# Kernel optimization log

Hardware: AMD Instinct MI355X
Metric: run time of the kernel (lower is better)

Reference implementation:

```python
import jax, jax.numpy as jnp
import numpy as np

B, MSG, H, D, N = 64, 64, 512, 512, 2048


def setup_inputs() -> dict:
    key = jax.random.key(0)
    ks = jax.random.split(key, 20)
    s = 0.02
    return {
        "message": jax.random.normal(ks[0], (B, MSG), jnp.float32),
        "state": jax.random.normal(ks[1], (B, H), jnp.float32),
        "image": jax.random.normal(ks[2], (B, H), jnp.float32),
        "class_descriptors": jax.random.normal(ks[3], (N, D), jnp.float32),
        # GRUCell params (torch layout: gates ordered r, z, n)
        "w_ih": jax.random.normal(ks[4], (3 * H, MSG), jnp.float32) * s,
        "w_hh": jax.random.normal(ks[5], (3 * H, H), jnp.float32) * s,
        "b_ih": jax.random.normal(ks[6], (3 * H,), jnp.float32) * s,
        "b_hh": jax.random.normal(ks[7], (3 * H,), jnp.float32) * s,
        "w_stop": jax.random.normal(ks[8], (1, H), jnp.float32) * s,
        "b_stop": jax.random.normal(ks[9], (1,), jnp.float32) * s,
        "w_y1": jax.random.normal(ks[10], (H, H + D), jnp.float32) * s,
        "b_y1": jax.random.normal(ks[11], (H,), jnp.float32) * s,
        "w_y2": jax.random.normal(ks[12], (1, H), jnp.float32) * s,
        "b_y2": jax.random.normal(ks[13], (1,), jnp.float32) * s,
        "w_state": jax.random.normal(ks[14], (H, H), jnp.float32) * s,
        "b_state": jax.random.normal(ks[15], (H,), jnp.float32) * s,
        "w_desc": jax.random.normal(ks[16], (H, D), jnp.float32) * s,  # no bias
        "w_msg": jax.random.normal(ks[17], (MSG, H), jnp.float32) * s,
        "b_msg": jax.random.normal(ks[18], (MSG,), jnp.float32) * s,
    }


def _gru_cell(x, h, w_ih, w_hh, b_ih, b_hh):
    gi = x @ w_ih.T + b_ih  # [B, 3H]
    gh = h @ w_hh.T + b_hh
    i_r, i_z, i_n = jnp.split(gi, 3, axis=1)
    h_r, h_z, h_n = jnp.split(gh, 3, axis=1)
    r = jax.nn.sigmoid(i_r + h_r)
    z = jax.nn.sigmoid(i_z + h_z)
    n = jnp.tanh(i_n + r * h_n)
    return (1.0 - z) * n + z * h


def reference(message, state, image, class_descriptors,
              w_ih, w_hh, b_ih, b_hh, w_stop, b_stop,
              w_y1, b_y1, w_y2, b_y2, w_state, b_state,
              w_desc, w_msg, b_msg):
    b, h = state.shape
    n, d = class_descriptors.shape

    new_state = _gru_cell(message, state, w_ih, w_hh, b_ih, b_hh)  # [B, H]
    stop_dist = jax.nn.sigmoid(new_state @ w_stop.T + b_stop)  # [B, 1]
    stop_bit = jax.lax.stop_gradient(jnp.round(stop_dist))  # eval-mode path

    # build_state_descriptor_pairs (faithful to torch view semantics,
    # including the (B, H, N) -> (B*N, H) interleaved reshape of pair_left)
    pair_left = jnp.broadcast_to(new_state[:, :, None], (b, h, n)).reshape(b * n, h)
    pair_right = jnp.broadcast_to(class_descriptors[None], (b, n, d)).reshape(b * n, d)
    pairs = jnp.concatenate([pair_left, pair_right], axis=1)  # [B*N, H+D]

    y = jnp.clip(pairs @ w_y1.T + b_y1, 0.0, None)  # relu, [B*N, H]
    y = (y @ w_y2.T + b_y2).reshape(b, -1)  # [B, N]
    y_scores = jax.lax.stop_gradient(jax.nn.softmax(y, axis=1))

    # reweight_descriptors: softmax-weighted sum over descriptors
    descriptor_influence = jnp.einsum('bn,nd->bd', y_scores, class_descriptors)

    message_state = jnp.tanh(new_state @ w_state.T + b_state
                             + descriptor_influence @ w_desc.T)
    message_dist = jax.nn.sigmoid(message_state @ w_msg.T + b_msg)  # [B, MSG]
    outp_msg = jax.lax.stop_gradient(jnp.round(message_dist))

    return stop_bit, stop_dist, outp_msg, message_dist, y
```

## Files before the change

kernel.cpp:

```cpp
#include <hip/hip_runtime.h>
#include <hip/hip_bf16.h>


__device__ __forceinline__ float sigm(float x) { return 1.0f / (1.0f + expf(-x)); }

__device__ __forceinline__ void stage_pad68(float* dst, const float* src, int c) {
  *(float4*)&dst[(c >> 4) * 68 + (c & 15) * 4] = *(const float4*)&src[c * 4];
}

__global__ __launch_bounds__(512) void gru_kernel(
    const float* __restrict__ msg, const float* __restrict__ st,
    const float* __restrict__ w_ih, const float* __restrict__ w_hh,
    const float* __restrict__ b_ih, const float* __restrict__ b_hh,
    float* __restrict__ ns, float* __restrict__ nsT) {
  const int h = blockIdx.x;
  const int t = threadIdx.x;
  __shared__ __align__(16) float sHr[544], sHz[544], sHn[544];
  __shared__ __align__(16) float sIr[64], sIz[64], sIn[64];
  if (t < 128)      stage_pad68(sHr, w_hh + h * 512, t);
  else if (t < 256) stage_pad68(sHz, w_hh + (h + 512) * 512, t - 128);
  else if (t < 384) stage_pad68(sHn, w_hh + (h + 1024) * 512, t - 256);
  else if (t < 400) ((float4*)sIr)[t - 384] = ((const float4*)(w_ih + h * 64))[t - 384];
  else if (t < 416) ((float4*)sIz)[t - 400] = ((const float4*)(w_ih + (h + 512) * 64))[t - 400];
  else if (t < 432) ((float4*)sIn)[t - 416] = ((const float4*)(w_ih + (h + 1024) * 64))[t - 416];
  __syncthreads();
  const int bi = t >> 3, kg = t & 7;
  float pr = 0.f, pz = 0.f, pin = 0.f, phn = 0.f;
  {
    const float* mrow = msg + bi * 64 + kg * 8;
    const float* ir = &sIr[kg * 8];
    const float* iz = &sIz[kg * 8];
    const float* in_ = &sIn[kg * 8];
    #pragma unroll
    for (int i = 0; i < 2; ++i) {
      float4 x = *(const float4*)&mrow[i * 4];
      float4 wr = *(const float4*)&ir[i * 4];
      float4 wz = *(const float4*)&iz[i * 4];
      float4 wn = *(const float4*)&in_[i * 4];
      pr = fmaf(x.x, wr.x, pr); pr = fmaf(x.y, wr.y, pr); pr = fmaf(x.z, wr.z, pr); pr = fmaf(x.w, wr.w, pr);
      pz = fmaf(x.x, wz.x, pz); pz = fmaf(x.y, wz.y, pz); pz = fmaf(x.z, wz.z, pz); pz = fmaf(x.w, wz.w, pz);
      pin = fmaf(x.x, wn.x, pin); pin = fmaf(x.y, wn.y, pin); pin = fmaf(x.z, wn.z, pin); pin = fmaf(x.w, wn.w, pin);
    }
  }
  {
    const float* srow = st + bi * 512 + kg * 64;
    const float* hr = &sHr[kg * 68];
    const float* hz = &sHz[kg * 68];
    const float* hn = &sHn[kg * 68];
    #pragma unroll
    for (int i = 0; i < 16; ++i) {
      float4 x = *(const float4*)&srow[i * 4];
      float4 wr = *(const float4*)&hr[i * 4];
      float4 wz = *(const float4*)&hz[i * 4];
      float4 wn = *(const float4*)&hn[i * 4];
      pr = fmaf(x.x, wr.x, pr); pr = fmaf(x.y, wr.y, pr); pr = fmaf(x.z, wr.z, pr); pr = fmaf(x.w, wr.w, pr);
      pz = fmaf(x.x, wz.x, pz); pz = fmaf(x.y, wz.y, pz); pz = fmaf(x.z, wz.z, pz); pz = fmaf(x.w, wz.w, pz);
      phn = fmaf(x.x, wn.x, phn); phn = fmaf(x.y, wn.y, phn); phn = fmaf(x.z, wn.z, phn); phn = fmaf(x.w, wn.w, phn);
    }
  }
  pr += __shfl_xor(pr, 1, 8); pr += __shfl_xor(pr, 2, 8); pr += __shfl_xor(pr, 4, 8);
  pz += __shfl_xor(pz, 1, 8); pz += __shfl_xor(pz, 2, 8); pz += __shfl_xor(pz, 4, 8);
  pin += __shfl_xor(pin, 1, 8); pin += __shfl_xor(pin, 2, 8); pin += __shfl_xor(pin, 4, 8);
  phn += __shfl_xor(phn, 1, 8); phn += __shfl_xor(phn, 2, 8); phn += __shfl_xor(phn, 4, 8);
  if ((t & 7) == 0) {
    float r = sigm(pr + b_ih[h] + b_hh[h]);
    float z = sigm(pz + b_ih[h + 512] + b_hh[h + 512]);
    float n = tanhf(pin + b_ih[h + 1024] + r * (phn + b_hh[h + 1024]));
    float hp = st[bi * 512 + h];
    float v = (1.0f - z) * n + z * hp;
    ns[bi * 512 + h] = v;
    nsT[h * 64 + bi] = v;
  }
}

__global__ __launch_bounds__(512) void stopws1_kernel(
    const float* __restrict__ w_y1, float* __restrict__ ws1,
    const float* __restrict__ ns, const float* __restrict__ w_stop,
    const float* __restrict__ b_stop, float* __restrict__ out_bit,
    float* __restrict__ out_dist) {
  const int t = threadIdx.x;
  if (blockIdx.x < 64) {
    const int j = blockIdx.x * 8 + (t >> 6);
    const int lane = t & 63;
    const float* row = w_y1 + j * 1024 + lane * 8;
    float4 a = *(const float4*)&row[0];
    float4 b = *(const float4*)&row[4];
    float acc = a.x + a.y + a.z + a.w + b.x + b.y + b.z + b.w;
    #pragma unroll
    for (int m = 1; m < 64; m <<= 1) acc += __shfl_xor(acc, m, 64);
    if (lane == 0) ws1[j] = acc;
  } else {
    const int bi = t >> 3, kg = t & 7;
    const float* row = ns + bi * 512 + kg * 64;
    const float* wrow = w_stop + kg * 64;
    float acc = 0.f;
    #pragma unroll
    for (int i = 0; i < 16; ++i) {
      float4 r = *(const float4*)&row[i * 4];
      float4 w = *(const float4*)&wrow[i * 4];
      acc = fmaf(r.x, w.x, acc); acc = fmaf(r.y, w.y, acc);
      acc = fmaf(r.z, w.z, acc); acc = fmaf(r.w, w.w, acc);
    }
    acc += __shfl_xor(acc, 1, 8); acc += __shfl_xor(acc, 2, 8); acc += __shfl_xor(acc, 4, 8);
    if ((t & 7) == 0) {
      float sd = sigm(acc + b_stop[0]);
      out_dist[bi] = sd;
      out_bit[bi] = rintf(sd);
    }
  }
}

#define GBK 16
__global__ __launch_bounds__(256) void g_kernel(
    const float* __restrict__ desc, const float* __restrict__ w_y1,
    const float* __restrict__ b_y1, const float* __restrict__ nsT,
    const float* __restrict__ ws1, const float* __restrict__ w_y2,
    float* __restrict__ yp) {
  __shared__ __align__(16) float As[GBK][64];
  __shared__ __align__(16) float Bs[GBK][64];
  __shared__ __align__(16) float sV[16][66];
  __shared__ __align__(16) float sW1[64], sW2[64];
  const int rr0 = blockIdx.x * 64;
  const int j0 = blockIdx.y * 64;
  const int tid = threadIdx.x;
  const int tm = (tid >> 4) * 4;
  const int tn = (tid & 15) * 4;
  const int lm = tid >> 2;
  const int lkq = (tid & 3) * 4;
  {
    const int q = tid >> 4, pos = (tid & 15) * 4;
    *(float4*)&sV[q][pos] = *(const float4*)&nsT[((rr0 >> 2) + q) * 64 + pos];
  }
  if (tid < 64) { sW1[tid] = ws1[j0 + tid]; sW2[tid] = w_y2[j0 + tid]; }
  float acc[4][4] = {};
  const float* aptr = desc + (rr0 + lm) * 512 + lkq;
  const float* bptr = w_y1 + (j0 + lm) * 1024 + 512 + lkq;
  float4 av = *(const float4*)aptr;
  float4 bv = *(const float4*)bptr;
  for (int k0 = 0; k0 < 512; k0 += GBK) {
    __syncthreads();
    As[lkq + 0][lm] = av.x; As[lkq + 1][lm] = av.y;
    As[lkq + 2][lm] = av.z; As[lkq + 3][lm] = av.w;
    Bs[lkq + 0][lm] = bv.x; Bs[lkq + 1][lm] = bv.y;
    Bs[lkq + 2][lm] = bv.z; Bs[lkq + 3][lm] = bv.w;
    __syncthreads();
    if (k0 + GBK < 512) {
      av = *(const float4*)(aptr + k0 + GBK);
      bv = *(const float4*)(bptr + k0 + GBK);
    }
    #pragma unroll
    for (int k = 0; k < GBK; ++k) {
      float4 a = *(const float4*)&As[k][tm];
      float4 b = *(const float4*)&Bs[k][tn];
      acc[0][0] = fmaf(a.x, b.x, acc[0][0]); acc[0][1] = fmaf(a.x, b.y, acc[0][1]);
      acc[0][2] = fmaf(a.x, b.z, acc[0][2]); acc[0][3] = fmaf(a.x, b.w, acc[0][3]);
      acc[1][0] = fmaf(a.y, b.x, acc[1][0]); acc[1][1] = fmaf(a.y, b.y, acc[1][1]);
      acc[1][2] = fmaf(a.y, b.z, acc[1][2]); acc[1][3] = fmaf(a.y, b.w, acc[1][3]);
      acc[2][0] = fmaf(a.z, b.x, acc[2][0]); acc[2][1] = fmaf(a.z, b.y, acc[2][1]);
      acc[2][2] = fmaf(a.z, b.z, acc[2][2]); acc[2][3] = fmaf(a.z, b.w, acc[2][3]);
      acc[3][0] = fmaf(a.w, b.x, acc[3][0]); acc[3][1] = fmaf(a.w, b.y, acc[3][1]);
      acc[3][2] = fmaf(a.w, b.z, acc[3][2]); acc[3][3] = fmaf(a.w, b.w, acc[3][3]);
    }
  }
  {
    float4 by = *(const float4*)&b_y1[j0 + tn];
    #pragma unroll
    for (int i = 0; i < 4; ++i) {
      acc[i][0] += by.x; acc[i][1] += by.y; acc[i][2] += by.z; acc[i][3] += by.w;
    }
  }
  const float4 w1 = *(const float4*)&sW1[tn];
  const float4 w2 = *(const float4*)&sW2[tn];
  const int vrow = tid >> 4;
  float* ypb = yp + blockIdx.y * 131072 + rr0 + tm;
  for (int bi = 0; bi < 64; ++bi) {
    const float v = sV[vrow][bi];
    float p0 = fmaf(w2.x, fmaxf(fmaf(v, w1.x, acc[0][0]), 0.f),
               fmaf(w2.y, fmaxf(fmaf(v, w1.y, acc[0][1]), 0.f),
               fmaf(w2.z, fmaxf(fmaf(v, w1.z, acc[0][2]), 0.f),
                    w2.w * fmaxf(fmaf(v, w1.w, acc[0][3]), 0.f))));
    float p1 = fmaf(w2.x, fmaxf(fmaf(v, w1.x, acc[1][0]), 0.f),
               fmaf(w2.y, fmaxf(fmaf(v, w1.y, acc[1][1]), 0.f),
               fmaf(w2.z, fmaxf(fmaf(v, w1.z, acc[1][2]), 0.f),
                    w2.w * fmaxf(fmaf(v, w1.w, acc[1][3]), 0.f))));
    float p2 = fmaf(w2.x, fmaxf(fmaf(v, w1.x, acc[2][0]), 0.f),
               fmaf(w2.y, fmaxf(fmaf(v, w1.y, acc[2][1]), 0.f),
               fmaf(w2.z, fmaxf(fmaf(v, w1.z, acc[2][2]), 0.f),
                    w2.w * fmaxf(fmaf(v, w1.w, acc[2][3]), 0.f))));
    float p3 = fmaf(w2.x, fmaxf(fmaf(v, w1.x, acc[3][0]), 0.f),
               fmaf(w2.y, fmaxf(fmaf(v, w1.y, acc[3][1]), 0.f),
               fmaf(w2.z, fmaxf(fmaf(v, w1.z, acc[3][2]), 0.f),
                    w2.w * fmaxf(fmaf(v, w1.w, acc[3][3]), 0.f))));
    p0 += __shfl_xor(p0, 1, 16); p0 += __shfl_xor(p0, 2, 16); p0 += __shfl_xor(p0, 4, 16); p0 += __shfl_xor(p0, 8, 16);
    p1 += __shfl_xor(p1, 1, 16); p1 += __shfl_xor(p1, 2, 16); p1 += __shfl_xor(p1, 4, 16); p1 += __shfl_xor(p1, 8, 16);
    p2 += __shfl_xor(p2, 1, 16); p2 += __shfl_xor(p2, 2, 16); p2 += __shfl_xor(p2, 4, 16); p2 += __shfl_xor(p2, 8, 16);
    p3 += __shfl_xor(p3, 1, 16); p3 += __shfl_xor(p3, 2, 16); p3 += __shfl_xor(p3, 4, 16); p3 += __shfl_xor(p3, 8, 16);
    if ((tid & 15) == 0) *(float4*)&ypb[bi * 2048] = make_float4(p0, p1, p2, p3);
  }
}

__global__ __launch_bounds__(256) void softmax_kernel(
    const float* __restrict__ yp, const float* __restrict__ b_y2,
    float* __restrict__ scores, float* __restrict__ out_y) {
  const int bi = blockIdx.x;
  const int t = threadIdx.x;
  __shared__ float sy[2048];
  __shared__ float red[256];
  const float b = b_y2[0];
  float lmax = -3.0e38f;
  for (int i = t; i < 2048; i += 256) {
    const float* p = yp + bi * 2048 + i;
    float v = b + p[0] + p[131072] + p[262144] + p[393216]
                + p[524288] + p[655360] + p[786432] + p[917504];
    sy[i] = v;
    out_y[bi * 2048 + i] = v;
    lmax = fmaxf(lmax, v);
  }
  red[t] = lmax;
  __syncthreads();
  for (int s = 128; s > 0; s >>= 1) {
    if (t < s) red[t] = fmaxf(red[t], red[t + s]);
    __syncthreads();
  }
  const float mx = red[0];
  __syncthreads();
  float lsum = 0.0f;
  for (int i = t; i < 2048; i += 256) {
    float e = expf(sy[i] - mx);
    sy[i] = e;
    lsum += e;
  }
  red[t] = lsum;
  __syncthreads();
  for (int s = 128; s > 0; s >>= 1) {
    if (t < s) red[t] += red[t + s];
    __syncthreads();
  }
  const float inv = 1.0f / red[0];
  for (int i = t; i < 2048; i += 256) scores[bi * 2048 + i] = sy[i] * inv;
}

__global__ __launch_bounds__(256) void di_part_kernel(
    const float* __restrict__ scores, const float* __restrict__ desc,
    float* __restrict__ dp) {
  __shared__ __align__(16) float sS[64][64];
  __shared__ __align__(16) float sD[64][64];
  const int d0 = blockIdx.x * 64;
  const int n0 = blockIdx.y * 64;
  const int tid = threadIdx.x;
  {
    const int bi = tid >> 2;
    #pragma unroll
    for (int i = 0; i < 4; ++i) {
      const int kq = (tid & 3) * 4 + i * 16;
      float4 av = *(const float4*)&scores[bi * 2048 + n0 + kq];
      sS[kq + 0][bi] = av.x; sS[kq + 1][bi] = av.y;
      sS[kq + 2][bi] = av.z; sS[kq + 3][bi] = av.w;
    }
  }
  {
    #pragma unroll
    for (int i = 0; i < 4; ++i) {
      const int nn = (tid >> 4) + i * 16;
      const int dq = (tid & 15) * 4;
      *(float4*)&sD[nn][dq] = *(const float4*)&desc[(n0 + nn) * 512 + d0 + dq];
    }
  }
  __syncthreads();
  const int bi0 = (tid >> 4) * 4;
  const int dd0 = (tid & 15) * 4;
  float acc[4][4] = {};
  #pragma unroll 8
  for (int nn = 0; nn < 64; ++nn) {
    float4 a = *(const float4*)&sS[nn][bi0];
    float4 b = *(const float4*)&sD[nn][dd0];
    acc[0][0] = fmaf(a.x, b.x, acc[0][0]); acc[0][1] = fmaf(a.x, b.y, acc[0][1]);
    acc[0][2] = fmaf(a.x, b.z, acc[0][2]); acc[0][3] = fmaf(a.x, b.w, acc[0][3]);
    acc[1][0] = fmaf(a.y, b.x, acc[1][0]); acc[1][1] = fmaf(a.y, b.y, acc[1][1]);
    acc[1][2] = fmaf(a.y, b.z, acc[1][2]); acc[1][3] = fmaf(a.y, b.w, acc[1][3]);
    acc[2][0] = fmaf(a.z, b.x, acc[2][0]); acc[2][1] = fmaf(a.z, b.y, acc[2][1]);
    acc[2][2] = fmaf(a.z, b.z, acc[2][2]); acc[2][3] = fmaf(a.z, b.w, acc[2][3]);
    acc[3][0] = fmaf(a.w, b.x, acc[3][0]); acc[3][1] = fmaf(a.w, b.y, acc[3][1]);
    acc[3][2] = fmaf(a.w, b.z, acc[3][2]); acc[3][3] = fmaf(a.w, b.w, acc[3][3]);
  }
  float* base = dp + blockIdx.y * 32768;
  #pragma unroll
  for (int i = 0; i < 4; ++i)
    #pragma unroll
    for (int j = 0; j < 4; ++j)
      base[(bi0 + i) * 512 + d0 + dd0 + j] = acc[i][j];
}

__global__ __launch_bounds__(512) void di_reduce_kernel(
    const float* __restrict__ dp, float* __restrict__ di) {
  const int idx = blockIdx.x * 512 + threadIdx.x;
  float acc = 0.0f;
  #pragma unroll 8
  for (int c = 0; c < 32; ++c) acc += dp[c * 32768 + idx];
  di[idx] = acc;
}

__global__ __launch_bounds__(512) void ms_kernel(
    const float* __restrict__ ns, const float* __restrict__ di,
    const float* __restrict__ w_state, const float* __restrict__ b_state,
    const float* __restrict__ w_desc, float* __restrict__ ms) {
  const int hj = blockIdx.x;
  const int t = threadIdx.x;
  __shared__ __align__(16) float sWs[544], sWd[544];
  if (t < 128)      stage_pad68(sWs, w_state + hj * 512, t);
  else if (t < 256) stage_pad68(sWd, w_desc + hj * 512, t - 128);
  __syncthreads();
  const int bi = t >> 3, kg = t & 7;
  const float* nr = ns + bi * 512 + kg * 64;
  const float* dr = di + bi * 512 + kg * 64;
  const float* wsp = &sWs[kg * 68];
  const float* wdp = &sWd[kg * 68];
  float acc = 0.f;
  #pragma unroll
  for (int i = 0; i < 16; ++i) {
    float4 a = *(const float4*)&nr[i * 4];
    float4 w = *(const float4*)&wsp[i * 4];
    float4 b = *(const float4*)&dr[i * 4];
    float4 u = *(const float4*)&wdp[i * 4];
    acc = fmaf(a.x, w.x, acc); acc = fmaf(a.y, w.y, acc);
    acc = fmaf(a.z, w.z, acc); acc = fmaf(a.w, w.w, acc);
    acc = fmaf(b.x, u.x, acc); acc = fmaf(b.y, u.y, acc);
    acc = fmaf(b.z, u.z, acc); acc = fmaf(b.w, u.w, acc);
  }
  acc += __shfl_xor(acc, 1, 8); acc += __shfl_xor(acc, 2, 8); acc += __shfl_xor(acc, 4, 8);
  if ((t & 7) == 0) ms[bi * 512 + hj] = tanhf(acc + b_state[hj]);
}

__global__ __launch_bounds__(512) void msg_kernel(
    const float* __restrict__ ms, const float* __restrict__ w_msg,
    const float* __restrict__ b_msg, float* __restrict__ out_msg,
    float* __restrict__ out_msgdist) {
  const int m = blockIdx.x;
  const int t = threadIdx.x;
  __shared__ __align__(16) float sW[544];
  if (t < 128) stage_pad68(sW, w_msg + m * 512, t);
  __syncthreads();
  const int bi = t >> 3, kg = t & 7;
  const float* row = ms + bi * 512 + kg * 64;
  const float* wp = &sW[kg * 68];
  float acc = 0.f;
  #pragma unroll
  for (int i = 0; i < 16; ++i) {
    float4 a = *(const float4*)&row[i * 4];
    float4 w = *(const float4*)&wp[i * 4];
    acc = fmaf(a.x, w.x, acc); acc = fmaf(a.y, w.y, acc);
    acc = fmaf(a.z, w.z, acc); acc = fmaf(a.w, w.w, acc);
  }
  acc += __shfl_xor(acc, 1, 8); acc += __shfl_xor(acc, 2, 8); acc += __shfl_xor(acc, 4, 8);
  if ((t & 7) == 0) {
    float md = sigm(acc + b_msg[m]);
    out_msgdist[bi * 64 + m] = md;
    out_msg[bi * 64 + m] = rintf(md);
  }
}

extern "C" void kernel_launch(void* const* d_in, const int* in_sizes, int n_in,
                              void* d_out, int out_size, void* d_ws, size_t ws_size,
                              hipStream_t stream) {
  (void)in_sizes; (void)n_in; (void)out_size; (void)ws_size;
  const float* message = (const float*)d_in[0];
  const float* state   = (const float*)d_in[1];
  const float* desc    = (const float*)d_in[3];
  const float* w_ih    = (const float*)d_in[4];
  const float* w_hh    = (const float*)d_in[5];
  const float* b_ih    = (const float*)d_in[6];
  const float* b_hh    = (const float*)d_in[7];
  const float* w_stop  = (const float*)d_in[8];
  const float* b_stop  = (const float*)d_in[9];
  const float* w_y1    = (const float*)d_in[10];
  const float* b_y1    = (const float*)d_in[11];
  const float* w_y2    = (const float*)d_in[12];
  const float* b_y2    = (const float*)d_in[13];
  const float* w_state = (const float*)d_in[14];
  const float* b_state = (const float*)d_in[15];
  const float* w_desc  = (const float*)d_in[16];
  const float* w_msg   = (const float*)d_in[17];
  const float* b_msg   = (const float*)d_in[18];

  float* out = (float*)d_out;
  float* out_stopbit  = out;
  float* out_stopdist = out + 64;
  float* out_msg      = out + 128;
  float* out_msgdist  = out + 4224;
  float* out_y        = out + 8320;

  char* ws = (char*)d_ws;
  float* ns     = (float*)(ws);
  float* nsT    = (float*)(ws + 131072);
  float* ws1    = (float*)(ws + 262144);
  float* yp     = (float*)(ws + 270336);
  float* scores = (float*)(ws + 4988928);
  float* di     = (float*)(ws + 5513216);
  float* ms     = (float*)(ws + 5644288);

  gru_kernel<<<512, 512, 0, stream>>>(message, state, w_ih, w_hh, b_ih, b_hh, ns, nsT);
  stopws1_kernel<<<65, 512, 0, stream>>>(w_y1, ws1, ns, w_stop, b_stop, out_stopbit, out_stopdist);
  g_kernel<<<dim3(32, 8), 256, 0, stream>>>(desc, w_y1, b_y1, nsT, ws1, w_y2, yp);
  softmax_kernel<<<64, 256, 0, stream>>>(yp, b_y2, scores, out_y);
  di_part_kernel<<<dim3(8, 32), 256, 0, stream>>>(scores, desc, yp);
  di_reduce_kernel<<<64, 512, 0, stream>>>(yp, di);
  ms_kernel<<<512, 512, 0, stream>>>(ns, di, w_state, b_state, w_desc, ms);
  msg_kernel<<<64, 512, 0, stream>>>(ms, w_msg, b_msg, out_msg, out_msgdist);
}
```

Measured before the change: 213.8 us.

## Fuse all stages into one persistent kernel with software grid barriers

Replaces the eight separate kernel launches with a single persistent 256-block kernel. The stages are separated by an atomic-counter grid barrier, and the barrier counter is reset each call with a memset. The goal is to remove launch gaps and per-kernel ramp-up. In exchange, phases that used 512 blocks now loop twice per block, the GEMM phase is retiled with 512 threads and its epilogue restructured, and correctness depends on all 256 blocks being co-resident.

```diff
diff --git a/kernel.cpp b/kernel.cpp
--- a/kernel.cpp
+++ b/kernel.cpp
@@ -1,6 +1,19 @@
 #include <hip/hip_runtime.h>
-#include <hip/hip_bf16.h>
-
+
+
+#define NBLK 256
+#define SMEM_FLOATS 9696
+
+struct Params {
+  const float *message, *state, *desc;
+  const float *w_ih, *w_hh, *b_ih, *b_hh;
+  const float *w_stop, *b_stop;
+  const float *w_y1, *b_y1, *w_y2, *b_y2;
+  const float *w_state, *b_state, *w_desc, *w_msg, *b_msg;
+  float *out_stopbit, *out_stopdist, *out_msg, *out_msgdist, *out_y;
+  float *ns, *nsT, *ws1, *yp, *scores, *di, *ms;
+  int *bar;
+};
 
 __device__ __forceinline__ float sigm(float x) { return 1.0f / (1.0f + expf(-x)); }
 
@@ -8,91 +21,108 @@
   *(float4*)&dst[(c >> 4) * 68 + (c & 15) * 4] = *(const float4*)&src[c * 4];
 }
 
-__global__ __launch_bounds__(512) void gru_kernel(
-    const float* __restrict__ msg, const float* __restrict__ st,
-    const float* __restrict__ w_ih, const float* __restrict__ w_hh,
-    const float* __restrict__ b_ih, const float* __restrict__ b_hh,
-    float* __restrict__ ns, float* __restrict__ nsT) {
-  const int h = blockIdx.x;
-  const int t = threadIdx.x;
-  __shared__ __align__(16) float sHr[544], sHz[544], sHn[544];
-  __shared__ __align__(16) float sIr[64], sIz[64], sIn[64];
-  if (t < 128)      stage_pad68(sHr, w_hh + h * 512, t);
-  else if (t < 256) stage_pad68(sHz, w_hh + (h + 512) * 512, t - 128);
-  else if (t < 384) stage_pad68(sHn, w_hh + (h + 1024) * 512, t - 256);
-  else if (t < 400) ((float4*)sIr)[t - 384] = ((const float4*)(w_ih + h * 64))[t - 384];
-  else if (t < 416) ((float4*)sIz)[t - 400] = ((const float4*)(w_ih + (h + 512) * 64))[t - 400];
-  else if (t < 432) ((float4*)sIn)[t - 416] = ((const float4*)(w_ih + (h + 1024) * 64))[t - 416];
-  __syncthreads();
-  const int bi = t >> 3, kg = t & 7;
-  float pr = 0.f, pz = 0.f, pin = 0.f, phn = 0.f;
-  {
-    const float* mrow = msg + bi * 64 + kg * 8;
-    const float* ir = &sIr[kg * 8];
-    const float* iz = &sIz[kg * 8];
-    const float* in_ = &sIn[kg * 8];
-    #pragma unroll
-    for (int i = 0; i < 2; ++i) {
-      float4 x = *(const float4*)&mrow[i * 4];
-      float4 wr = *(const float4*)&ir[i * 4];
-      float4 wz = *(const float4*)&iz[i * 4];
-      float4 wn = *(const float4*)&in_[i * 4];
-      pr = fmaf(x.x, wr.x, pr); pr = fmaf(x.y, wr.y, pr); pr = fmaf(x.z, wr.z, pr); pr = fmaf(x.w, wr.w, pr);
-      pz = fmaf(x.x, wz.x, pz); pz = fmaf(x.y, wz.y, pz); pz = fmaf(x.z, wz.z, pz); pz = fmaf(x.w, wz.w, pz);
-      pin = fmaf(x.x, wn.x, pin); pin = fmaf(x.y, wn.y, pin); pin = fmaf(x.z, wn.z, pin); pin = fmaf(x.w, wn.w, pin);
-    }
-  }
-  {
-    const float* srow = st + bi * 512 + kg * 64;
-    const float* hr = &sHr[kg * 68];
-    const float* hz = &sHz[kg * 68];
-    const float* hn = &sHn[kg * 68];
-    #pragma unroll
-    for (int i = 0; i < 16; ++i) {
-      float4 x = *(const float4*)&srow[i * 4];
-      float4 wr = *(const float4*)&hr[i * 4];
-      float4 wz = *(const float4*)&hz[i * 4];
-      float4 wn = *(const float4*)&hn[i * 4];
-      pr = fmaf(x.x, wr.x, pr); pr = fmaf(x.y, wr.y, pr); pr = fmaf(x.z, wr.z, pr); pr = fmaf(x.w, wr.w, pr);
-      pz = fmaf(x.x, wz.x, pz); pz = fmaf(x.y, wz.y, pz); pz = fmaf(x.z, wz.z, pz); pz = fmaf(x.w, wz.w, pz);
-      phn = fmaf(x.x, wn.x, phn); phn = fmaf(x.y, wn.y, phn); phn = fmaf(x.z, wn.z, phn); phn = fmaf(x.w, wn.w, phn);
-    }
-  }
-  pr += __shfl_xor(pr, 1, 8); pr += __shfl_xor(pr, 2, 8); pr += __shfl_xor(pr, 4, 8);
-  pz += __shfl_xor(pz, 1, 8); pz += __shfl_xor(pz, 2, 8); pz += __shfl_xor(pz, 4, 8);
-  pin += __shfl_xor(pin, 1, 8); pin += __shfl_xor(pin, 2, 8); pin += __shfl_xor(pin, 4, 8);
-  phn += __shfl_xor(phn, 1, 8); phn += __shfl_xor(phn, 2, 8); phn += __shfl_xor(phn, 4, 8);
-  if ((t & 7) == 0) {
-    float r = sigm(pr + b_ih[h] + b_hh[h]);
-    float z = sigm(pz + b_ih[h + 512] + b_hh[h + 512]);
-    float n = tanhf(pin + b_ih[h + 1024] + r * (phn + b_hh[h + 1024]));
-    float hp = st[bi * 512 + h];
-    float v = (1.0f - z) * n + z * hp;
-    ns[bi * 512 + h] = v;
-    nsT[h * 64 + bi] = v;
-  }
-}
-
-__global__ __launch_bounds__(512) void stopws1_kernel(
-    const float* __restrict__ w_y1, float* __restrict__ ws1,
-    const float* __restrict__ ns, const float* __restrict__ w_stop,
-    const float* __restrict__ b_stop, float* __restrict__ out_bit,
-    float* __restrict__ out_dist) {
-  const int t = threadIdx.x;
-  if (blockIdx.x < 64) {
-    const int j = blockIdx.x * 8 + (t >> 6);
+__device__ __forceinline__ void grid_barrier(int* bar) {
+  __syncthreads();
+  __threadfence();
+  if (threadIdx.x == 0) {
+    int* cnt = bar;
+    int* gen = bar + 1;
+    int g = __hip_atomic_load(gen, __ATOMIC_ACQUIRE, __HIP_MEMORY_SCOPE_AGENT);
+    int a = __hip_atomic_fetch_add(cnt, 1, __ATOMIC_ACQ_REL, __HIP_MEMORY_SCOPE_AGENT);
+    if (a == NBLK - 1) {
+      __hip_atomic_store(cnt, 0, __ATOMIC_RELAXED, __HIP_MEMORY_SCOPE_AGENT);
+      __hip_atomic_store(gen, g + 1, __ATOMIC_RELEASE, __HIP_MEMORY_SCOPE_AGENT);
+    } else {
+      while (__hip_atomic_load(gen, __ATOMIC_ACQUIRE, __HIP_MEMORY_SCOPE_AGENT) == g) {
+        __builtin_amdgcn_s_sleep(2);
+      }
+    }
+  }
+  __syncthreads();
+}
+
+__device__ void phase_gru(const Params& P, float* sm, int blk, int t) {
+  float* sHr = sm;
+  float* sHz = sm + 544;
+  float* sHn = sm + 1088;
+  float* sIr = sm + 1632;
+  float* sIz = sm + 1696;
+  float* sIn = sm + 1760;
+  for (int pass = 0; pass < 2; ++pass) {
+    const int h = blk + pass * 256;
+    __syncthreads();
+    if (t < 128)      stage_pad68(sHr, P.w_hh + h * 512, t);
+    else if (t < 256) stage_pad68(sHz, P.w_hh + (h + 512) * 512, t - 128);
+    else if (t < 384) stage_pad68(sHn, P.w_hh + (h + 1024) * 512, t - 256);
+    else if (t < 400) ((float4*)sIr)[t - 384] = ((const float4*)(P.w_ih + h * 64))[t - 384];
+    else if (t < 416) ((float4*)sIz)[t - 400] = ((const float4*)(P.w_ih + (h + 512) * 64))[t - 400];
+    else if (t < 432) ((float4*)sIn)[t - 416] = ((const float4*)(P.w_ih + (h + 1024) * 64))[t - 416];
+    __syncthreads();
+    const int bi = t >> 3, kg = t & 7;
+    float pr = 0.f, pz = 0.f, pin = 0.f, phn = 0.f;
+    {
+      const float* mrow = P.message + bi * 64 + kg * 8;
+      const float* ir = &sIr[kg * 8];
+      const float* iz = &sIz[kg * 8];
+      const float* in_ = &sIn[kg * 8];
+      #pragma unroll
+      for (int i = 0; i < 2; ++i) {
+        float4 x = *(const float4*)&mrow[i * 4];
+        float4 wr = *(const float4*)&ir[i * 4];
+        float4 wz = *(const float4*)&iz[i * 4];
+        float4 wn = *(const float4*)&in_[i * 4];
+        pr = fmaf(x.x, wr.x, pr); pr = fmaf(x.y, wr.y, pr); pr = fmaf(x.z, wr.z, pr); pr = fmaf(x.w, wr.w, pr);
+        pz = fmaf(x.x, wz.x, pz); pz = fmaf(x.y, wz.y, pz); pz = fmaf(x.z, wz.z, pz); pz = fmaf(x.w, wz.w, pz);
+        pin = fmaf(x.x, wn.x, pin); pin = fmaf(x.y, wn.y, pin); pin = fmaf(x.z, wn.z, pin); pin = fmaf(x.w, wn.w, pin);
+      }
+    }
+    {
+      const float* srow = P.state + bi * 512 + kg * 64;
+      const float* hr = &sHr[kg * 68];
+      const float* hz = &sHz[kg * 68];
+      const float* hn = &sHn[kg * 68];
+      #pragma unroll
+      for (int i = 0; i < 16; ++i) {
+        float4 x = *(const float4*)&srow[i * 4];
+        float4 wr = *(const float4*)&hr[i * 4];
+        float4 wz = *(const float4*)&hz[i * 4];
+        float4 wn = *(const float4*)&hn[i * 4];
+        pr = fmaf(x.x, wr.x, pr); pr = fmaf(x.y, wr.y, pr); pr = fmaf(x.z, wr.z, pr); pr = fmaf(x.w, wr.w, pr);
+        pz = fmaf(x.x, wz.x, pz); pz = fmaf(x.y, wz.y, pz); pz = fmaf(x.z, wz.z, pz); pz = fmaf(x.w, wz.w, pz);
+        phn = fmaf(x.x, wn.x, phn); phn = fmaf(x.y, wn.y, phn); phn = fmaf(x.z, wn.z, phn); phn = fmaf(x.w, wn.w, phn);
+      }
+    }
+    pr += __shfl_xor(pr, 1, 8); pr += __shfl_xor(pr, 2, 8); pr += __shfl_xor(pr, 4, 8);
+    pz += __shfl_xor(pz, 1, 8); pz += __shfl_xor(pz, 2, 8); pz += __shfl_xor(pz, 4, 8);
+    pin += __shfl_xor(pin, 1, 8); pin += __shfl_xor(pin, 2, 8); pin += __shfl_xor(pin, 4, 8);
+    phn += __shfl_xor(phn, 1, 8); phn += __shfl_xor(phn, 2, 8); phn += __shfl_xor(phn, 4, 8);
+    if ((t & 7) == 0) {
+      float r = sigm(pr + P.b_ih[h] + P.b_hh[h]);
+      float z = sigm(pz + P.b_ih[h + 512] + P.b_hh[h + 512]);
+      float n = tanhf(pin + P.b_ih[h + 1024] + r * (phn + P.b_hh[h + 1024]));
+      float hp = P.state[bi * 512 + h];
+      float v = (1.0f - z) * n + z * hp;
+      P.ns[bi * 512 + h] = v;
+      P.nsT[h * 64 + bi] = v;
+    }
+  }
+}
+
+__device__ void phase_stopws1(const Params& P, int blk, int t) {
+  if (blk < 64) {
+    const int j = blk * 8 + (t >> 6);
     const int lane = t & 63;
-    const float* row = w_y1 + j * 1024 + lane * 8;
+    const float* row = P.w_y1 + j * 1024 + lane * 8;
     float4 a = *(const float4*)&row[0];
     float4 b = *(const float4*)&row[4];
     float acc = a.x + a.y + a.z + a.w + b.x + b.y + b.z + b.w;
     #pragma unroll
     for (int m = 1; m < 64; m <<= 1) acc += __shfl_xor(acc, m, 64);
-    if (lane == 0) ws1[j] = acc;
-  } else {
+    if (lane == 0) P.ws1[j] = acc;
+  } else if (blk == 64) {
     const int bi = t >> 3, kg = t & 7;
-    const float* row = ns + bi * 512 + kg * 64;
-    const float* wrow = w_stop + kg * 64;
+    const float* row = P.ns + bi * 512 + kg * 64;
+    const float* wrow = P.w_stop + kg * 64;
     float acc = 0.f;
     #pragma unroll
     for (int i = 0; i < 16; ++i) {
@@ -103,245 +133,203 @@
     }
     acc += __shfl_xor(acc, 1, 8); acc += __shfl_xor(acc, 2, 8); acc += __shfl_xor(acc, 4, 8);
     if ((t & 7) == 0) {
-      float sd = sigm(acc + b_stop[0]);
-      out_dist[bi] = sd;
-      out_bit[bi] = rintf(sd);
-    }
-  }
-}
-
-#define GBK 16
-__global__ __launch_bounds__(256) void g_kernel(
-    const float* __restrict__ desc, const float* __restrict__ w_y1,
-    const float* __restrict__ b_y1, const float* __restrict__ nsT,
-    const float* __restrict__ ws1, const float* __restrict__ w_y2,
-    float* __restrict__ yp) {
-  __shared__ __align__(16) float As[GBK][64];
-  __shared__ __align__(16) float Bs[GBK][64];
-  __shared__ __align__(16) float sV[16][66];
-  __shared__ __align__(16) float sW1[64], sW2[64];
-  const int rr0 = blockIdx.x * 64;
-  const int j0 = blockIdx.y * 64;
-  const int tid = threadIdx.x;
-  const int tm = (tid >> 4) * 4;
-  const int tn = (tid & 15) * 4;
-  const int lm = tid >> 2;
-  const int lkq = (tid & 3) * 4;
-  {
-    const int q = tid >> 4, pos = (tid & 15) * 4;
-    *(float4*)&sV[q][pos] = *(const float4*)&nsT[((rr0 >> 2) + q) * 64 + pos];
-  }
-  if (tid < 64) { sW1[tid] = ws1[j0 + tid]; sW2[tid] = w_y2[j0 + tid]; }
-  float acc[4][4] = {};
-  const float* aptr = desc + (rr0 + lm) * 512 + lkq;
-  const float* bptr = w_y1 + (j0 + lm) * 1024 + 512 + lkq;
+      float sd = sigm(acc + P.b_stop[0]);
+      P.out_stopdist[bi] = sd;
+      P.out_stopbit[bi] = rintf(sd);
+    }
+  }
+}
+
+__device__ void phase_g(const Params& P, float* sm, int blk, int t) {
+  float* As  = sm;
+  float* Bs  = sm + 2176;
+  float* Gt  = sm + 4352;
+  float* sV  = sm + 8512;
+  float* sW1 = sm + 9568;
+  float* sW2 = sm + 9632;
+  const int rr0 = (blk >> 3) * 64;
+  const int j0  = (blk & 7) * 64;
+  if (t < 256) {
+    const int q = t >> 4, pos = (t & 15) * 4;
+    *(float4*)&sV[q * 66 + pos] = *(const float4*)&P.nsT[((rr0 >> 2) + q) * 64 + pos];
+  }
+  if (t < 64) { sW1[t] = P.ws1[j0 + t]; sW2[t] = P.w_y2[j0 + t]; }
+  const int lm = t >> 3, lk4 = (t & 7) * 4;
+  const int tm2 = (t >> 4) * 2;
+  const int tn4 = (t & 15) * 4;
+  const float* aptr = P.desc + (rr0 + lm) * 512 + lk4;
+  const float* bptr = P.w_y1 + (j0 + lm) * 1024 + 512 + lk4;
   float4 av = *(const float4*)aptr;
   float4 bv = *(const float4*)bptr;
-  for (int k0 = 0; k0 < 512; k0 += GBK) {
-    __syncthreads();
-    As[lkq + 0][lm] = av.x; As[lkq + 1][lm] = av.y;
-    As[lkq + 2][lm] = av.z; As[lkq + 3][lm] = av.w;
-    Bs[lkq + 0][lm] = bv.x; Bs[lkq + 1][lm] = bv.y;
-    Bs[lkq + 2][lm] = bv.z; Bs[lkq + 3][lm] = bv.w;
-    __syncthreads();
-    if (k0 + GBK < 512) {
-      av = *(const float4*)(aptr + k0 + GBK);
-      bv = *(const float4*)(bptr + k0 + GBK);
+  float acc[2][4] = {};
+  for (int k0 = 0; k0 < 512; k0 += 32) {
+    __syncthreads();
+    As[(lk4 + 0) * 68 + lm] = av.x; As[(lk4 + 1) * 68 + lm] = av.y;
+    As[(lk4 + 2) * 68 + lm] = av.z; As[(lk4 + 3) * 68 + lm] = av.w;
+    Bs[(lk4 + 0) * 68 + lm] = bv.x; Bs[(lk4 + 1) * 68 + lm] = bv.y;
+    Bs[(lk4 + 2) * 68 + lm] = bv.z; Bs[(lk4 + 3) * 68 + lm] = bv.w;
+    __syncthreads();
+    if (k0 + 32 < 512) {
+      av = *(const float4*)(aptr + k0 + 32);
+      bv = *(const float4*)(bptr + k0 + 32);
     }
     #pragma unroll
-    for (int k = 0; k < GBK; ++k) {
-      float4 a = *(const float4*)&As[k][tm];
-      float4 b = *(const float4*)&Bs[k][tn];
+    for (int k = 0; k < 32; ++k) {
+      float2 a = *(const float2*)&As[k * 68 + tm2];
+      float4 b = *(const float4*)&Bs[k * 68 + tn4];
       acc[0][0] = fmaf(a.x, b.x, acc[0][0]); acc[0][1] = fmaf(a.x, b.y, acc[0][1]);
       acc[0][2] = fmaf(a.x, b.z, acc[0][2]); acc[0][3] = fmaf(a.x, b.w, acc[0][3]);
       acc[1][0] = fmaf(a.y, b.x, acc[1][0]); acc[1][1] = fmaf(a.y, b.y, acc[1][1]);
       acc[1][2] = fmaf(a.y, b.z, acc[1][2]); acc[1][3] = fmaf(a.y, b.w, acc[1][3]);
-      acc[2][0] = fmaf(a.z, b.x, acc[2][0]); acc[2][1] = fmaf(a.z, b.y, acc[2][1]);
-      acc[2][2] = fmaf(a.z, b.z, acc[2][2]); acc[2][3] = fmaf(a.z, b.w, acc[2][3]);
-      acc[3][0] = fmaf(a.w, b.x, acc[3][0]); acc[3][1] = fmaf(a.w, b.y, acc[3][1]);
-      acc[3][2] = fmaf(a.w, b.z, acc[3][2]); acc[3][3] = fmaf(a.w, b.w, acc[3][3]);
     }
   }
   {
-    float4 by = *(const float4*)&b_y1[j0 + tn];
+    float4 by = *(const float4*)&P.b_y1[j0 + tn4];
+    acc[0][0] += by.x; acc[0][1] += by.y; acc[0][2] += by.z; acc[0][3] += by.w;
+    acc[1][0] += by.x; acc[1][1] += by.y; acc[1][2] += by.z; acc[1][3] += by.w;
+  }
+  #pragma unroll
+  for (int jj = 0; jj < 4; ++jj) {
+    Gt[(tn4 + jj) * 65 + tm2 + 0] = acc[0][jj];
+    Gt[(tn4 + jj) * 65 + tm2 + 1] = acc[1][jj];
+  }
+  __syncthreads();
+  const int rr = t & 63, g8 = t >> 6;
+  float v[8], p[8];
+  #pragma unroll
+  for (int q = 0; q < 8; ++q) { v[q] = sV[(rr >> 2) * 66 + g8 + q * 8]; p[q] = 0.f; }
+  #pragma unroll 4
+  for (int j = 0; j < 64; ++j) {
+    float gv = Gt[j * 65 + rr];
+    float w1j = sW1[j], w2j = sW2[j];
     #pragma unroll
-    for (int i = 0; i < 4; ++i) {
-      acc[i][0] += by.x; acc[i][1] += by.y; acc[i][2] += by.z; acc[i][3] += by.w;
-    }
-  }
-  const float4 w1 = *(const float4*)&sW1[tn];
-  const float4 w2 = *(const float4*)&sW2[tn];
-  const int vrow = tid >> 4;
-  float* ypb = yp + blockIdx.y * 131072 + rr0 + tm;
-  for (int bi = 0; bi < 64; ++bi) {
-    const float v = sV[vrow][bi];
-    float p0 = fmaf(w2.x, fmaxf(fmaf(v, w1.x, acc[0][0]), 0.f),
-               fmaf(w2.y, fmaxf(fmaf(v, w1.y, acc[0][1]), 0.f),
-               fmaf(w2.z, fmaxf(fmaf(v, w1.z, acc[0][2]), 0.f),
-                    w2.w * fmaxf(fmaf(v, w1.w, acc[0][3]), 0.f))));
-    float p1 = fmaf(w2.x, fmaxf(fmaf(v, w1.x, acc[1][0]), 0.f),
-               fmaf(w2.y, fmaxf(fmaf(v, w1.y, acc[1][1]), 0.f),
-               fmaf(w2.z, fmaxf(fmaf(v, w1.z, acc[1][2]), 0.f),
-                    w2.w * fmaxf(fmaf(v, w1.w, acc[1][3]), 0.f))));
-    float p2 = fmaf(w2.x, fmaxf(fmaf(v, w1.x, acc[2][0]), 0.f),
-               fmaf(w2.y, fmaxf(fmaf(v, w1.y, acc[2][1]), 0.f),
-               fmaf(w2.z, fmaxf(fmaf(v, w1.z, acc[2][2]), 0.f),
-                    w2.w * fmaxf(fmaf(v, w1.w, acc[2][3]), 0.f))));
-    float p3 = fmaf(w2.x, fmaxf(fmaf(v, w1.x, acc[3][0]), 0.f),
-               fmaf(w2.y, fmaxf(fmaf(v, w1.y, acc[3][1]), 0.f),
-               fmaf(w2.z, fmaxf(fmaf(v, w1.z, acc[3][2]), 0.f),
-                    w2.w * fmaxf(fmaf(v, w1.w, acc[3][3]), 0.f))));
-    p0 += __shfl_xor(p0, 1, 16); p0 += __shfl_xor(p0, 2, 16); p0 += __shfl_xor(p0, 4, 16); p0 += __shfl_xor(p0, 8, 16);
-    p1 += __shfl_xor(p1, 1, 16); p1 += __shfl_xor(p1, 2, 16); p1 += __shfl_xor(p1, 4, 16); p1 += __shfl_xor(p1, 8, 16);
-    p2 += __shfl_xor(p2, 1, 16); p2 += __shfl_xor(p2, 2, 16); p2 += __shfl_xor(p2, 4, 16); p2 += __shfl_xor(p2, 8, 16);
-    p3 += __shfl_xor(p3, 1, 16); p3 += __shfl_xor(p3, 2, 16); p3 += __shfl_xor(p3, 4, 16); p3 += __shfl_xor(p3, 8, 16);
-    if ((tid & 15) == 0) *(float4*)&ypb[bi * 2048] = make_float4(p0, p1, p2, p3);
-  }
-}
-
-__global__ __launch_bounds__(256) void softmax_kernel(
-    const float* __restrict__ yp, const float* __restrict__ b_y2,
-    float* __restrict__ scores, float* __restrict__ out_y) {
-  const int bi = blockIdx.x;
-  const int t = threadIdx.x;
-  __shared__ float sy[2048];
-  __shared__ float red[256];
-  const float b = b_y2[0];
+    for (int q = 0; q < 8; ++q)
+      p[q] = fmaf(w2j, fmaxf(fmaf(v[q], w1j, gv), 0.f), p[q]);
+  }
+  float* ypb = P.yp + (blk & 7) * 131072 + rr0 + rr;
+  #pragma unroll
+  for (int q = 0; q < 8; ++q) ypb[(g8 + q * 8) * 2048] = p[q];
+}
+
+__device__ void phase_softmax(const Params& P, float* sm, int blk, int t) {
+  if (blk >= 64) return;
+  float* sy = sm;
+  float* red = sm + 2048;
+  const int bi = blk;
+  const float b = P.b_y2[0];
   float lmax = -3.0e38f;
-  for (int i = t; i < 2048; i += 256) {
-    const float* p = yp + bi * 2048 + i;
+  for (int i = t; i < 2048; i += 512) {
+    const float* p = P.yp + bi * 2048 + i;
     float v = b + p[0] + p[131072] + p[262144] + p[393216]
                 + p[524288] + p[655360] + p[786432] + p[917504];
     sy[i] = v;
-    out_y[bi * 2048 + i] = v;
+    P.out_y[bi * 2048 + i] = v;
     lmax = fmaxf(lmax, v);
   }
   red[t] = lmax;
   __syncthreads();
-  for (int s = 128; s > 0; s >>= 1) {
+  for (int s = 256; s > 0; s >>= 1) {
     if (t < s) red[t] = fmaxf(red[t], red[t + s]);
     __syncthreads();
   }
   const float mx = red[0];
   __syncthreads();
   float lsum = 0.0f;
-  for (int i = t; i < 2048; i += 256) {
+  for (int i = t; i < 2048; i += 512) {
     float e = expf(sy[i] - mx);
     sy[i] = e;
     lsum += e;
   }
   red[t] = lsum;
   __syncthreads();
-  for (int s = 128; s > 0; s >>= 1) {
+  for (int s = 256; s > 0; s >>= 1) {
     if (t < s) red[t] += red[t + s];
     __syncthreads();
   }
   const float inv = 1.0f / red[0];
-  for (int i = t; i < 2048; i += 256) scores[bi * 2048 + i] = sy[i] * inv;
-}
-
-__global__ __launch_bounds__(256) void di_part_kernel(
-    const float* __restrict__ scores, const float* __restrict__ desc,
-    float* __restrict__ dp) {
-  __shared__ __align__(16) float sS[64][64];
-  __shared__ __align__(16) float sD[64][64];
-  const int d0 = blockIdx.x * 64;
-  const int n0 = blockIdx.y * 64;
-  const int tid = threadIdx.x;
+  for (int i = t; i < 2048; i += 512) P.scores[bi * 2048 + i] = sy[i] * inv;
+}
+
+__device__ void phase_dipart(const Params& P, float* sm, int blk, int t) {
+  float* sS = sm;
+  float* sD = sm + 4224;
+  const int d0 = (blk >> 5) * 64;
+  const int n0 = (blk & 31) * 64;
   {
-    const int bi = tid >> 2;
-    #pragma unroll
-    for (int i = 0; i < 4; ++i) {
-      const int kq = (tid & 3) * 4 + i * 16;
-      float4 av = *(const float4*)&scores[bi * 2048 + n0 + kq];
-      sS[kq + 0][bi] = av.x; sS[kq + 1][bi] = av.y;
-      sS[kq + 2][bi] = av.z; sS[kq + 3][bi] = av.w;
-    }
-  }
-  {
-    #pragma unroll
-    for (int i = 0; i < 4; ++i) {
-      const int nn = (tid >> 4) + i * 16;
-      const int dq = (tid & 15) * 4;
-      *(float4*)&sD[nn][dq] = *(const float4*)&desc[(n0 + nn) * 512 + d0 + dq];
-    }
-  }
-  __syncthreads();
-  const int bi0 = (tid >> 4) * 4;
-  const int dd0 = (tid & 15) * 4;
-  float acc[4][4] = {};
+    const int bi_s = t >> 3, q8 = (t & 7) * 8;
+    float4 s0 = *(const float4*)&P.scores[bi_s * 2048 + n0 + q8];
+    float4 s1 = *(const float4*)&P.scores[bi_s * 2048 + n0 + q8 + 4];
+    sS[(q8 + 0) * 66 + bi_s] = s0.x; sS[(q8 + 1) * 66 + bi_s] = s0.y;
+    sS[(q8 + 2) * 66 + bi_s] = s0.z; sS[(q8 + 3) * 66 + bi_s] = s0.w;
+    sS[(q8 + 4) * 66 + bi_s] = s1.x; sS[(q8 + 5) * 66 + bi_s] = s1.y;
+    sS[(q8 + 6) * 66 + bi_s] = s1.z; sS[(q8 + 7) * 66 + bi_s] = s1.w;
+    *(float4*)&sD[bi_s * 68 + q8]     = *(const float4*)&P.desc[(n0 + bi_s) * 512 + d0 + q8];
+    *(float4*)&sD[bi_s * 68 + q8 + 4] = *(const float4*)&P.desc[(n0 + bi_s) * 512 + d0 + q8 + 4];
+  }
+  __syncthreads();
+  const int bi0 = (t >> 4) * 2, dd0 = (t & 15) * 4;
+  float acc[2][4] = {};
   #pragma unroll 8
   for (int nn = 0; nn < 64; ++nn) {
-    float4 a = *(const float4*)&sS[nn][bi0];
-    float4 b = *(const float4*)&sD[nn][dd0];
+    float2 a = *(const float2*)&sS[nn * 66 + bi0];
+    float4 b = *(const float4*)&sD[nn * 68 + dd0];
     acc[0][0] = fmaf(a.x, b.x, acc[0][0]); acc[0][1] = fmaf(a.x, b.y, acc[0][1]);
     acc[0][2] = fmaf(a.x, b.z, acc[0][2]); acc[0][3] = fmaf(a.x, b.w, acc[0][3]);
     acc[1][0] = fmaf(a.y, b.x, acc[1][0]); acc[1][1] = fmaf(a.y, b.y, acc[1][1]);
     acc[1][2] = fmaf(a.y, b.z, acc[1][2]); acc[1][3] = fmaf(a.y, b.w, acc[1][3]);
-    acc[2][0] = fmaf(a.z, b.x, acc[2][0]); acc[2][1] = fmaf(a.z, b.y, acc[2][1]);
-    acc[2][2] = fmaf(a.z, b.z, acc[2][2]); acc[2][3] = fmaf(a.z, b.w, acc[2][3]);
-    acc[3][0] = fmaf(a.w, b.x, acc[3][0]); acc[3][1] = fmaf(a.w, b.y, acc[3][1]);
-    acc[3][2] = fmaf(a.w, b.z, acc[3][2]); acc[3][3] = fmaf(a.w, b.w, acc[3][3]);
-  }
-  float* base = dp + blockIdx.y * 32768;
-  #pragma unroll
-  for (int i = 0; i < 4; ++i)
-    #pragma unroll
-    for (int j = 0; j < 4; ++j)
-      base[(bi0 + i) * 512 + d0 + dd0 + j] = acc[i][j];
-}
-
-__global__ __launch_bounds__(512) void di_reduce_kernel(
-    const float* __restrict__ dp, float* __restrict__ di) {
-  const int idx = blockIdx.x * 512 + threadIdx.x;
+  }
+  float* base = P.yp + (blk & 31) * 32768;
+  *(float4*)&base[(bi0 + 0) * 512 + d0 + dd0] = make_float4(acc[0][0], acc[0][1], acc[0][2], acc[0][3]);
+  *(float4*)&base[(bi0 + 1) * 512 + d0 + dd0] = make_float4(acc[1][0], acc[1][1], acc[1][2], acc[1][3]);
+}
+
+__device__ void phase_direduce(const Params& P, int blk, int t) {
+  if (blk >= 64) return;
+  const int idx = blk * 512 + t;
   float acc = 0.0f;
   #pragma unroll 8
-  for (int c = 0; c < 32; ++c) acc += dp[c * 32768 + idx];
-  di[idx] = acc;
-}
-
-__global__ __launch_bounds__(512) void ms_kernel(
-    const float* __restrict__ ns, const float* __restrict__ di,
-    const float* __restrict__ w_state, const float* __restrict__ b_state,
-    const float* __restrict__ w_desc, float* __restrict__ ms) {
-  const int hj = blockIdx.x;
-  const int t = threadIdx.x;
-  __shared__ __align__(16) float sWs[544], sWd[544];
-  if (t < 128)      stage_pad68(sWs, w_state + hj * 512, t);
-  else if (t < 256) stage_pad68(sWd, w_desc + hj * 512, t - 128);
+  for (int c = 0; c < 32; ++c) acc += P.yp[c * 32768 + idx];
+  P.di[idx] = acc;
+}
+
+__device__ void phase_ms(const Params& P, float* sm, int blk, int t) {
+  float* sWs = sm;
+  float* sWd = sm + 544;
+  for (int pass = 0; pass < 2; ++pass) {
+    const int hj = blk + pass * 256;
+    __syncthreads();
+    if (t < 128)      stage_pad68(sWs, P.w_state + hj * 512, t);
+    else if (t < 256) stage_pad68(sWd, P.w_desc + hj * 512, t - 128);
+    __syncthreads();
+    const int bi = t >> 3, kg = t & 7;
+    const float* nr = P.ns + bi * 512 + kg * 64;
+    const float* dr = P.di + bi * 512 + kg * 64;
+    const float* wsp = &sWs[kg * 68];
+    const float* wdp = &sWd[kg * 68];
+    float acc = 0.f;
+    #pragma unroll
+    for (int i = 0; i < 16; ++i) {
+      float4 a = *(const float4*)&nr[i * 4];
+      float4 w = *(const float4*)&wsp[i * 4];
+      float4 b = *(const float4*)&dr[i * 4];
+      float4 u = *(const float4*)&wdp[i * 4];
+      acc = fmaf(a.x, w.x, acc); acc = fmaf(a.y, w.y, acc);
+      acc = fmaf(a.z, w.z, acc); acc = fmaf(a.w, w.w, acc);
+      acc = fmaf(b.x, u.x, acc); acc = fmaf(b.y, u.y, acc);
+      acc = fmaf(b.z, u.z, acc); acc = fmaf(b.w, u.w, acc);
+    }
+    acc += __shfl_xor(acc, 1, 8); acc += __shfl_xor(acc, 2, 8); acc += __shfl_xor(acc, 4, 8);
+    if ((t & 7) == 0) P.ms[bi * 512 + hj] = tanhf(acc + P.b_state[hj]);
+  }
+}
+
+__device__ void phase_msg(const Params& P, float* sm, int blk, int t) {
+  if (blk >= 64) return;
+  float* sW = sm;
+  if (t < 128) stage_pad68(sW, P.w_msg + blk * 512, t);
   __syncthreads();
   const int bi = t >> 3, kg = t & 7;
-  const float* nr = ns + bi * 512 + kg * 64;
-  const float* dr = di + bi * 512 + kg * 64;
-  const float* wsp = &sWs[kg * 68];
-  const float* wdp = &sWd[kg * 68];
-  float acc = 0.f;
-  #pragma unroll
-  for (int i = 0; i < 16; ++i) {
-    float4 a = *(const float4*)&nr[i * 4];
-    float4 w = *(const float4*)&wsp[i * 4];
-    float4 b = *(const float4*)&dr[i * 4];
-    float4 u = *(const float4*)&wdp[i * 4];
-    acc = fmaf(a.x, w.x, acc); acc = fmaf(a.y, w.y, acc);
-    acc = fmaf(a.z, w.z, acc); acc = fmaf(a.w, w.w, acc);
-    acc = fmaf(b.x, u.x, acc); acc = fmaf(b.y, u.y, acc);
-    acc = fmaf(b.z, u.z, acc); acc = fmaf(b.w, u.w, acc);
-  }
-  acc += __shfl_xor(acc, 1, 8); acc += __shfl_xor(acc, 2, 8); acc += __shfl_xor(acc, 4, 8);
-  if ((t & 7) == 0) ms[bi * 512 + hj] = tanhf(acc + b_state[hj]);
-}
-
-__global__ __launch_bounds__(512) void msg_kernel(
-    const float* __restrict__ ms, const float* __restrict__ w_msg,
-    const float* __restrict__ b_msg, float* __restrict__ out_msg,
-    float* __restrict__ out_msgdist) {
-  const int m = blockIdx.x;
-  const int t = threadIdx.x;
-  __shared__ __align__(16) float sW[544];
-  if (t < 128) stage_pad68(sW, w_msg + m * 512, t);
-  __syncthreads();
-  const int bi = t >> 3, kg = t & 7;
-  const float* row = ms + bi * 512 + kg * 64;
+  const float* row = P.ms + bi * 512 + kg * 64;
   const float* wp = &sW[kg * 68];
   float acc = 0.f;
   #pragma unroll
@@ -353,57 +341,74 @@
   }
   acc += __shfl_xor(acc, 1, 8); acc += __shfl_xor(acc, 2, 8); acc += __shfl_xor(acc, 4, 8);
   if ((t & 7) == 0) {
-    float md = sigm(acc + b_msg[m]);
-    out_msgdist[bi * 64 + m] = md;
-    out_msg[bi * 64 + m] = rintf(md);
-  }
+    float md = sigm(acc + P.b_msg[blk]);
+    P.out_msgdist[bi * 64 + blk] = md;
+    P.out_msg[bi * 64 + blk] = rintf(md);
+  }
+}
+
+__global__ __launch_bounds__(512, 1) void fused_kernel(Params P) {
+  __shared__ float sm[SMEM_FLOATS];
+  const int blk = blockIdx.x, t = threadIdx.x;
+  phase_gru(P, sm, blk, t);
+  grid_barrier(P.bar);
+  phase_stopws1(P, blk, t);
+  grid_barrier(P.bar);
+  phase_g(P, sm, blk, t);
+  grid_barrier(P.bar);
+  phase_softmax(P, sm, blk, t);
+  grid_barrier(P.bar);
+  phase_dipart(P, sm, blk, t);
+  grid_barrier(P.bar);
+  phase_direduce(P, blk, t);
+  grid_barrier(P.bar);
+  phase_ms(P, sm, blk, t);
+  grid_barrier(P.bar);
+  phase_msg(P, sm, blk, t);
 }
 
 extern "C" void kernel_launch(void* const* d_in, const int* in_sizes, int n_in,
                               void* d_out, int out_size, void* d_ws, size_t ws_size,
                               hipStream_t stream) {
   (void)in_sizes; (void)n_in; (void)out_size; (void)ws_size;
-  const float* message = (const float*)d_in[0];
-  const float* state   = (const float*)d_in[1];
-  const float* desc    = (const float*)d_in[3];
-  const float* w_ih    = (const float*)d_in[4];
-  const float* w_hh    = (const float*)d_in[5];
-  const float* b_ih    = (const float*)d_in[6];
-  const float* b_hh    = (const float*)d_in[7];
-  const float* w_stop  = (const float*)d_in[8];
-  const float* b_stop  = (const float*)d_in[9];
-  const float* w_y1    = (const float*)d_in[10];
-  const float* b_y1    = (const float*)d_in[11];
-  const float* w_y2    = (const float*)d_in[12];
-  const float* b_y2    = (const float*)d_in[13];
-  const float* w_state = (const float*)d_in[14];
-  const float* b_state = (const float*)d_in[15];
-  const float* w_desc  = (const float*)d_in[16];
-  const float* w_msg   = (const float*)d_in[17];
-  const float* b_msg   = (const float*)d_in[18];
-
   float* out = (float*)d_out;
-  float* out_stopbit  = out;
-  float* out_stopdist = out + 64;
-  float* out_msg      = out + 128;
-  float* out_msgdist  = out + 4224;
-  float* out_y        = out + 8320;
-
   char* ws = (char*)d_ws;
-  float* ns     = (float*)(ws);
-  float* nsT    = (float*)(ws + 131072);
-  float* ws1    = (float*)(ws + 262144);
-  float* yp     = (float*)(ws + 270336);
-  float* scores = (float*)(ws + 4988928);
-  float* di     = (float*)(ws + 5513216);
-  float* ms     = (float*)(ws + 5644288);
-
-  gru_kernel<<<512, 512, 0, stream>>>(message, state, w_ih, w_hh, b_ih, b_hh, ns, nsT);
-  stopws1_kernel<<<65, 512, 0, stream>>>(w_y1, ws1, ns, w_stop, b_stop, out_stopbit, out_stopdist);
-  g_kernel<<<dim3(32, 8), 256, 0, stream>>>(desc, w_y1, b_y1, nsT, ws1, w_y2, yp);
-  softmax_kernel<<<64, 256, 0, stream>>>(yp, b_y2, scores, out_y);
-  di_part_kernel<<<dim3(8, 32), 256, 0, stream>>>(scores, desc, yp);
-  di_reduce_kernel<<<64, 512, 0, stream>>>(yp, di);
-  ms_kernel<<<512, 512, 0, stream>>>(ns, di, w_state, b_state, w_desc, ms);
-  msg_kernel<<<64, 512, 0, stream>>>(ms, w_msg, b_msg, out_msg, out_msgdist);
-}
+
+  Params p;
+  p.message = (const float*)d_in[0];
+  p.state   = (const float*)d_in[1];
+  p.desc    = (const float*)d_in[3];
+  p.w_ih    = (const float*)d_in[4];
+  p.w_hh    = (const float*)d_in[5];
+  p.b_ih    = (const float*)d_in[6];
+  p.b_hh    = (const float*)d_in[7];
+  p.w_stop  = (const float*)d_in[8];
+  p.b_stop  = (const float*)d_in[9];
+  p.w_y1    = (const float*)d_in[10];
+  p.b_y1    = (const float*)d_in[11];
+  p.w_y2    = (const float*)d_in[12];
+  p.b_y2    = (const float*)d_in[13];
+  p.w_state = (const float*)d_in[14];
+  p.b_state = (const float*)d_in[15];
+  p.w_desc  = (const float*)d_in[16];
+  p.w_msg   = (const float*)d_in[17];
+  p.b_msg   = (const float*)d_in[18];
+
+  p.out_stopbit  = out;
+  p.out_stopdist = out + 64;
+  p.out_msg      = out + 128;
+  p.out_msgdist  = out + 4224;
+  p.out_y        = out + 8320;
+
+  p.ns     = (float*)(ws);
+  p.nsT    = (float*)(ws + 131072);
+  p.ws1    = (float*)(ws + 262144);
+  p.yp     = (float*)(ws + 270336);
+  p.scores = (float*)(ws + 4988928);
+  p.di     = (float*)(ws + 5513216);
+  p.ms     = (float*)(ws + 5644288);
+  p.bar    = (int*)(ws + 5775360);
+
+  hipMemsetAsync(p.bar, 0, 2 * sizeof(int), stream);
+  fused_kernel<<<NBLK, 512, 0, stream>>>(p);
+}
```

Result: slower. 578.9 us (+170.8%).
